# Kernel optimization log

Hardware: AMD Instinct MI355X
Metric: run time of the kernel (lower is better)

The kernel has to match this reference:

```python
import jax, jax.numpy as jnp
import numpy as np

N_NODES = 50000
N_EDGES = 500000
D_NODE = 128
D_EDGE = 128
HIDDEN = 64


def setup_inputs() -> dict:
    key = jax.random.key(0)
    k = jax.random.split(key, 8)
    x = jax.random.normal(k[0], (N_NODES, D_NODE), dtype=jnp.float32)
    edge_index = jax.random.randint(k[1], (2, N_EDGES), 0, N_NODES, dtype=jnp.int64)
    e = jax.random.normal(k[2], (N_EDGES, D_EDGE), dtype=jnp.float32)
    d_in = 2 * D_NODE + D_EDGE
    # Kaiming-uniform-ish init like torch Linear
    W1 = jax.random.uniform(k[3], (d_in, HIDDEN), jnp.float32, -1.0, 1.0) / np.sqrt(d_in)
    b1 = jax.random.uniform(k[4], (HIDDEN,), jnp.float32, -1.0, 1.0) / np.sqrt(d_in)
    W2 = jax.random.uniform(k[5], (HIDDEN, D_EDGE), jnp.float32, -1.0, 1.0) / np.sqrt(HIDDEN)
    b2 = jax.random.uniform(k[6], (D_EDGE,), jnp.float32, -1.0, 1.0) / np.sqrt(HIDDEN)
    return {"x": x, "edge_index": edge_index, "e": e,
            "W1": W1, "b1": b1, "W2": W2, "b2": b2}


def reference(x, edge_index, e, W1, b1, W2, b2):
    src = edge_index[0]
    dst = edge_index[1]
    # gather node features for each edge endpoint: [E, d_node] each
    inp = jnp.concatenate([x[src], x[dst], e], axis=-1)  # [E, 2*d_node + d_edge]
    h = jax.nn.relu(inp @ W1 + b1)                       # [E, hidden]
    return e + (h @ W2 + b2)                             # residual edge update [E, d_edge]
```

## Files before the change

### kernel.cpp

```cpp
#include <hip/hip_runtime.h>

#define EN   500000
#define DN   128
#define DIN  384
#define HID  64
#define NTILES 31250

typedef __attribute__((ext_vector_type(8))) short bf16x8;
typedef __attribute__((ext_vector_type(4))) float f32x4;

__device__ __forceinline__ short f2bf(float f) {
    union { float f; unsigned u; } v; v.f = f;
    return (short)((v.u + 0x7FFFu + ((v.u >> 16) & 1u)) >> 16);
}

__global__ void prep_weights(const float* __restrict__ W1, const float* __restrict__ W2,
                             short* __restrict__ W1T, short* __restrict__ W2T) {
    int i = blockIdx.x * 256 + threadIdx.x;
    if (i < DIN * HID) {
        int k = i / HID, n = i % HID;
        W1T[n * DIN + k] = f2bf(W1[i]);
    }
    if (i < HID * DN) {
        int k = i / DN, d = i % DN;
        W2T[d * HID + k] = f2bf(W2[i]);
    }
}

__global__ __launch_bounds__(256, 3)
void edge_update(const float* __restrict__ x, const int* __restrict__ ei,
                 const float* __restrict__ e, const float* __restrict__ b1,
                 const float* __restrict__ b2, const short* __restrict__ W1T,
                 const short* __restrict__ W2T, float* __restrict__ out) {
    __shared__ short hbuf[4][16 * 72];

    const int tid  = threadIdx.x;
    const int wave = tid >> 6;
    const int lane = tid & 63;
    const int m    = lane & 15;
    const int q    = lane >> 4;
    const int kq   = q * 8;

    short* hb = &hbuf[wave][0];

    for (int t = 0; t < 2; ++t) {
        const int tile = blockIdx.x * 8 + wave * 2 + t;
        if (tile >= NTILES) continue;
        const int ebase = tile * 16;
        const int edge  = ebase + m;

        const int src = ei[edge];
        const int dst = ei[EN + edge];
        const float* rsrc = x + (size_t)src  * DN;
        const float* rdst = x + (size_t)dst  * DN;
        const float* rede = e + (size_t)edge * DN;

        f32x4 acc1[4];
        #pragma unroll
        for (int nt = 0; nt < 4; ++nt) acc1[nt] = (f32x4){0.f, 0.f, 0.f, 0.f};

        #pragma unroll
        for (int reg = 0; reg < 3; ++reg) {
            const float* rp = (reg == 0) ? rsrc : (reg == 1) ? rdst : rede;
            #pragma unroll
            for (int ks = 0; ks < 4; ++ks) {
                const float* ap = rp + ks * 32 + kq;
                f32x4 v0 = *(const f32x4*)ap;
                f32x4 v1 = *(const f32x4*)(ap + 4);
                bf16x8 a;
                a[0] = f2bf(v0[0]); a[1] = f2bf(v0[1]); a[2] = f2bf(v0[2]); a[3] = f2bf(v0[3]);
                a[4] = f2bf(v1[0]); a[5] = f2bf(v1[1]); a[6] = f2bf(v1[2]); a[7] = f2bf(v1[3]);
                const int kglob = (reg * 4 + ks) * 32 + kq;
                #pragma unroll
                for (int nt = 0; nt < 4; ++nt) {
                    bf16x8 b = *(const bf16x8*)(W1T + (m + 16 * nt) * DIN + kglob);
                    acc1[nt] = __builtin_amdgcn_mfma_f32_16x16x32_bf16(a, b, acc1[nt], 0, 0, 0);
                }
            }
        }

        #pragma unroll
        for (int nt = 0; nt < 4; ++nt) {
            const int col = m + 16 * nt;
            const float bv = b1[col];
            #pragma unroll
            for (int r = 0; r < 4; ++r) {
                float h = acc1[nt][r] + bv;
                h = h > 0.f ? h : 0.f;
                hb[(q * 4 + r) * 72 + col] = f2bf(h);
            }
        }

        bf16x8 a0 = *(const bf16x8*)(hb + m * 72 + kq);
        bf16x8 a1 = *(const bf16x8*)(hb + m * 72 + 32 + kq);

        f32x4 acc2[8];
        #pragma unroll
        for (int nt = 0; nt < 8; ++nt) acc2[nt] = (f32x4){0.f, 0.f, 0.f, 0.f};

        #pragma unroll
        for (int nt = 0; nt < 8; ++nt) {
            const short* wp = W2T + (m + 16 * nt) * HID + kq;
            bf16x8 b0 = *(const bf16x8*)wp;
            bf16x8 b1v = *(const bf16x8*)(wp + 32);
            acc2[nt] = __builtin_amdgcn_mfma_f32_16x16x32_bf16(a0, b0,  acc2[nt], 0, 0, 0);
            acc2[nt] = __builtin_amdgcn_mfma_f32_16x16x32_bf16(a1, b1v, acc2[nt], 0, 0, 0);
        }

        #pragma unroll
        for (int nt = 0; nt < 8; ++nt) {
            const int d = m + 16 * nt;
            const float bv = b2[d];
            #pragma unroll
            for (int r = 0; r < 4; ++r) {
                const size_t idx = (size_t)(ebase + q * 4 + r) * DN + d;
                out[idx] = e[idx] + acc2[nt][r] + bv;
            }
        }
    }
}

extern "C" void kernel_launch(void* const* d_in, const int* in_sizes, int n_in,
                              void* d_out, int out_size, void* d_ws, size_t ws_size,
                              hipStream_t stream) {
    const float* x  = (const float*)d_in[0];
    const int*   ei = (const int*)d_in[1];
    const float* e  = (const float*)d_in[2];
    const float* W1 = (const float*)d_in[3];
    const float* b1 = (const float*)d_in[4];
    const float* W2 = (const float*)d_in[5];
    const float* b2 = (const float*)d_in[6];
    float* out = (float*)d_out;

    short* W1T = (short*)d_ws;
    short* W2T = W1T + HID * DIN;

    prep_weights<<<96, 256, 0, stream>>>(W1, W2, W1T, W2T);

    const int nblocks = (NTILES + 7) / 8;
    edge_update<<<nblocks, 256, 0, stream>>>(x, ei, e, b1, b2, W1T, W2T, out);
}
```

Baseline: 695.6 us.

## Pre-convert node features to bf16 and stage edge features in LDS for residual

Adds a pre-pass that converts x to a bf16 copy in workspace, so the per-edge src/dst gathers read half the bytes and skip repeated conversion. Edge features are loaded once, kept in LDS, and reused for the residual add instead of being re-read from global memory. The cost is an extra kernel launch, about 13MB of workspace, and more LDS per block, which could limit occupancy. If the workspace is too small, it falls back to the fp32 gather path.

```diff
diff --git a/kernel.cpp b/kernel.cpp
--- a/kernel.cpp
+++ b/kernel.cpp
@@ -1,10 +1,12 @@
 #include <hip/hip_runtime.h>
 
+#define NN   50000
 #define EN   500000
 #define DN   128
 #define DIN  384
 #define HID  64
 #define NTILES 31250
+#define EST  132
 
 typedef __attribute__((ext_vector_type(8))) short bf16x8;
 typedef __attribute__((ext_vector_type(4))) float f32x4;
@@ -27,11 +29,26 @@
     }
 }
 
+__global__ void prep_x(const float* __restrict__ x, short* __restrict__ xb) {
+    int i = blockIdx.x * 256 + threadIdx.x;
+    if (i >= NN * DN / 8) return;
+    const float* p = x + (size_t)i * 8;
+    f32x4 v0 = *(const f32x4*)p;
+    f32x4 v1 = *(const f32x4*)(p + 4);
+    bf16x8 o;
+    o[0] = f2bf(v0[0]); o[1] = f2bf(v0[1]); o[2] = f2bf(v0[2]); o[3] = f2bf(v0[3]);
+    o[4] = f2bf(v1[0]); o[5] = f2bf(v1[1]); o[6] = f2bf(v1[2]); o[7] = f2bf(v1[3]);
+    *(bf16x8*)(xb + (size_t)i * 8) = o;
+}
+
+template<bool XB>
 __global__ __launch_bounds__(256, 3)
-void edge_update(const float* __restrict__ x, const int* __restrict__ ei,
-                 const float* __restrict__ e, const float* __restrict__ b1,
-                 const float* __restrict__ b2, const short* __restrict__ W1T,
-                 const short* __restrict__ W2T, float* __restrict__ out) {
+void edge_update(const float* __restrict__ x, const short* __restrict__ xb,
+                 const int* __restrict__ ei, const float* __restrict__ e,
+                 const float* __restrict__ b1, const float* __restrict__ b2,
+                 const short* __restrict__ W1T, const short* __restrict__ W2T,
+                 float* __restrict__ out) {
+    __shared__ float ebuf[4][16 * EST];
     __shared__ short hbuf[4][16 * 72];
 
     const int tid  = threadIdx.x;
@@ -41,6 +58,7 @@
     const int q    = lane >> 4;
     const int kq   = q * 8;
 
+    float* eb = &ebuf[wave][0];
     short* hb = &hbuf[wave][0];
 
     for (int t = 0; t < 2; ++t) {
@@ -51,31 +69,66 @@
 
         const int src = ei[edge];
         const int dst = ei[EN + edge];
-        const float* rsrc = x + (size_t)src  * DN;
-        const float* rdst = x + (size_t)dst  * DN;
-        const float* rede = e + (size_t)edge * DN;
+
+        bf16x8 as[4], ad[4], ae[4];
+        if (XB) {
+            const short* ps = xb + (size_t)src * DN;
+            const short* pd = xb + (size_t)dst * DN;
+            #pragma unroll
+            for (int ks = 0; ks < 4; ++ks) {
+                as[ks] = *(const bf16x8*)(ps + ks * 32 + kq);
+                ad[ks] = *(const bf16x8*)(pd + ks * 32 + kq);
+            }
+        } else {
+            const float* rs = x + (size_t)src * DN;
+            const float* rd = x + (size_t)dst * DN;
+            #pragma unroll
+            for (int ks = 0; ks < 4; ++ks) {
+                f32x4 s0 = *(const f32x4*)(rs + ks * 32 + kq);
+                f32x4 s1 = *(const f32x4*)(rs + ks * 32 + kq + 4);
+                f32x4 d0 = *(const f32x4*)(rd + ks * 32 + kq);
+                f32x4 d1 = *(const f32x4*)(rd + ks * 32 + kq + 4);
+                bf16x8 a, b;
+                a[0]=f2bf(s0[0]); a[1]=f2bf(s0[1]); a[2]=f2bf(s0[2]); a[3]=f2bf(s0[3]);
+                a[4]=f2bf(s1[0]); a[5]=f2bf(s1[1]); a[6]=f2bf(s1[2]); a[7]=f2bf(s1[3]);
+                b[0]=f2bf(d0[0]); b[1]=f2bf(d0[1]); b[2]=f2bf(d0[2]); b[3]=f2bf(d0[3]);
+                b[4]=f2bf(d1[0]); b[5]=f2bf(d1[1]); b[6]=f2bf(d1[2]); b[7]=f2bf(d1[3]);
+                as[ks] = a; ad[ks] = b;
+            }
+        }
+
+        const float* re = e + (size_t)edge * DN;
+        f32x4 ev[8];
+        #pragma unroll
+        for (int ks = 0; ks < 4; ++ks) {
+            ev[2*ks]   = *(const f32x4*)(re + ks * 32 + kq);
+            ev[2*ks+1] = *(const f32x4*)(re + ks * 32 + kq + 4);
+        }
+        #pragma unroll
+        for (int ks = 0; ks < 4; ++ks) {
+            *(f32x4*)(eb + m * EST + ks * 32 + kq)     = ev[2*ks];
+            *(f32x4*)(eb + m * EST + ks * 32 + kq + 4) = ev[2*ks+1];
+        }
+        #pragma unroll
+        for (int ks = 0; ks < 4; ++ks) {
+            bf16x8 a;
+            a[0]=f2bf(ev[2*ks][0]); a[1]=f2bf(ev[2*ks][1]); a[2]=f2bf(ev[2*ks][2]); a[3]=f2bf(ev[2*ks][3]);
+            a[4]=f2bf(ev[2*ks+1][0]); a[5]=f2bf(ev[2*ks+1][1]); a[6]=f2bf(ev[2*ks+1][2]); a[7]=f2bf(ev[2*ks+1][3]);
+            ae[ks] = a;
+        }
 
         f32x4 acc1[4];
         #pragma unroll
         for (int nt = 0; nt < 4; ++nt) acc1[nt] = (f32x4){0.f, 0.f, 0.f, 0.f};
 
         #pragma unroll
-        for (int reg = 0; reg < 3; ++reg) {
-            const float* rp = (reg == 0) ? rsrc : (reg == 1) ? rdst : rede;
-            #pragma unroll
-            for (int ks = 0; ks < 4; ++ks) {
-                const float* ap = rp + ks * 32 + kq;
-                f32x4 v0 = *(const f32x4*)ap;
-                f32x4 v1 = *(const f32x4*)(ap + 4);
-                bf16x8 a;
-                a[0] = f2bf(v0[0]); a[1] = f2bf(v0[1]); a[2] = f2bf(v0[2]); a[3] = f2bf(v0[3]);
-                a[4] = f2bf(v1[0]); a[5] = f2bf(v1[1]); a[6] = f2bf(v1[2]); a[7] = f2bf(v1[3]);
-                const int kglob = (reg * 4 + ks) * 32 + kq;
-                #pragma unroll
-                for (int nt = 0; nt < 4; ++nt) {
-                    bf16x8 b = *(const bf16x8*)(W1T + (m + 16 * nt) * DIN + kglob);
-                    acc1[nt] = __builtin_amdgcn_mfma_f32_16x16x32_bf16(a, b, acc1[nt], 0, 0, 0);
-                }
+        for (int ks = 0; ks < 12; ++ks) {
+            bf16x8 a = (ks < 4) ? as[ks] : (ks < 8) ? ad[ks - 4] : ae[ks - 8];
+            const int kglob = ks * 32 + kq;
+            #pragma unroll
+            for (int nt = 0; nt < 4; ++nt) {
+                bf16x8 b = *(const bf16x8*)(W1T + (m + 16 * nt) * DIN + kglob);
+                acc1[nt] = __builtin_amdgcn_mfma_f32_16x16x32_bf16(a, b, acc1[nt], 0, 0, 0);
             }
         }
 
@@ -101,7 +154,7 @@
         #pragma unroll
         for (int nt = 0; nt < 8; ++nt) {
             const short* wp = W2T + (m + 16 * nt) * HID + kq;
-            bf16x8 b0 = *(const bf16x8*)wp;
+            bf16x8 b0  = *(const bf16x8*)wp;
             bf16x8 b1v = *(const bf16x8*)(wp + 32);
             acc2[nt] = __builtin_amdgcn_mfma_f32_16x16x32_bf16(a0, b0,  acc2[nt], 0, 0, 0);
             acc2[nt] = __builtin_amdgcn_mfma_f32_16x16x32_bf16(a1, b1v, acc2[nt], 0, 0, 0);
@@ -113,8 +166,8 @@
             const float bv = b2[d];
             #pragma unroll
             for (int r = 0; r < 4; ++r) {
-                const size_t idx = (size_t)(ebase + q * 4 + r) * DN + d;
-                out[idx] = e[idx] + acc2[nt][r] + bv;
+                const int row = q * 4 + r;
+                out[(size_t)(ebase + row) * DN + d] = eb[row * EST + d] + acc2[nt][r] + bv;
             }
         }
     }
@@ -134,9 +187,16 @@
 
     short* W1T = (short*)d_ws;
     short* W2T = W1T + HID * DIN;
+    short* xb  = W2T + HID * DN;
+    const size_t need_xb = (size_t)(HID * DIN + HID * DN + NN * DN) * 2;
 
     prep_weights<<<96, 256, 0, stream>>>(W1, W2, W1T, W2T);
 
     const int nblocks = (NTILES + 7) / 8;
-    edge_update<<<nblocks, 256, 0, stream>>>(x, ei, e, b1, b2, W1T, W2T, out);
-}
+    if (ws_size >= need_xb) {
+        prep_x<<<(NN * DN / 8 + 255) / 256, 256, 0, stream>>>(x, xb);
+        edge_update<true><<<nblocks, 256, 0, stream>>>(x, xb, ei, e, b1, b2, W1T, W2T, out);
+    } else {
+        edge_update<false><<<nblocks, 256, 0, stream>>>(x, xb, ei, e, b1, b2, W1T, W2T, out);
+    }
+}
```

Result: faster. 672.5 us (-3.3%).
